# Kernel optimization log

Hardware: AMD Instinct MI355X
Metric: run time of the kernel (lower is better)

## Reference

```python
import jax, jax.numpy as jnp
import numpy as np

FACTOR = 5

def setup_inputs() -> dict:
    key = jax.random.key(0)
    k1, k2, k3, k4 = jax.random.split(key, 4)
    B, L, H, D = 4, 2048, 8, 64
    sample_k = min(FACTOR * int(np.ceil(np.log(L))), L)  # 40
    return {
        "queries": jax.random.normal(k1, (B, L, H, D), dtype=jnp.float32),
        "keys": jax.random.normal(k2, (B, L, H, D), dtype=jnp.float32),
        "values": jax.random.normal(k3, (B, L, H, D), dtype=jnp.float32),
        "index_sample": jax.random.randint(k4, (L, sample_k), 0, L, dtype=jnp.int32),
    }

def reference(queries, keys, values, index_sample):
    # [B, L, H, D] -> [B, H, L, D]
    Q = jnp.transpose(queries, (0, 2, 1, 3))
    K = jnp.transpose(keys, (0, 2, 1, 3))
    V = jnp.transpose(values, (0, 2, 1, 3))
    B, H, L_Q, D = Q.shape
    L_K = K.shape[2]
    u = min(FACTOR * int(np.ceil(np.log(L_Q))), L_Q)  # n_top

    # --- _prob_QK: sampled QK scores ---
    # K_sample: [B, H, L_Q, sample_k, D]
    K_sample = K[:, :, index_sample, :]
    # Q_K_sample[b,h,l,s] = Q[b,h,l,:] . K_sample[b,h,l,s,:]
    Q_K_sample = jnp.einsum('bhld,bhlsd->bhls', Q, K_sample)
    # sparsity measure M: max - mean over L_K
    M = Q_K_sample.max(axis=-1) - Q_K_sample.sum(axis=-1) / L_K  # [B,H,L_Q]
    _, M_top = jax.lax.top_k(M, u)  # [B,H,u]

    # reduced Q -> full scores against all keys
    Q_reduce = jnp.take_along_axis(Q, M_top[..., None], axis=2)  # [B,H,u,D]
    scores = jnp.einsum('bhud,bhkd->bhuk', Q_reduce, K)  # [B,H,u,L_K]
    scale = 1.0 / jnp.sqrt(jnp.asarray(D, dtype=scores.dtype))
    scores = scores * scale

    # --- initial context: mean of V over keys (mask_flag=False) ---
    V_mean = V.mean(axis=-2)  # [B,H,D]
    context = jnp.broadcast_to(V_mean[:, :, None, :], (B, H, L_Q, D))

    # --- update context at top-u query positions ---
    attn = jax.nn.softmax(scores, axis=-1)  # [B,H,u,L_K]
    ctx_top = jnp.einsum('bhuk,bhkd->bhud', attn, V)  # [B,H,u,D]
    b_idx = jnp.arange(B)[:, None, None]
    h_idx = jnp.arange(H)[None, :, None]
    context = context.at[b_idx, h_idx, M_top].set(ctx_top)
    return context  # [B, H, L_Q, D]
```

## Files before the change

### kernel.cpp

```cpp
#include <hip/hip_runtime.h>
#include <math.h>

#define LL 2048
#define HH 8
#define DD 64
#define SK 40
#define UU 40
#define SCALE 0.125f


__global__ __launch_bounds__(512) void k_m(
    const float* __restrict__ Q, const float* __restrict__ K,
    const int* __restrict__ idxs, float* __restrict__ Mout)
{
  int bx = blockIdx.x;
  int b = bx >> 11, l = bx & (LL - 1);
  int t = threadIdx.x;
  int h = t >> 6, lane = t & 63;
  int sg = lane >> 2, dg = lane & 3;

  const float* qrow = Q + (((size_t)(b * LL + l) * HH + h) << 6);
  float4 qv[4];
#pragma unroll
  for (int i = 0; i < 4; ++i)
    qv[i] = *(const float4*)(qrow + i * 16 + dg * 4);

  const int* ip = idxs + l * SK;
  float mx = -INFINITY, sum = 0.f;

#pragma unroll
  for (int c = 0; c < 3; ++c) {
    int s = c * 16 + sg;
    int idx = (s < SK) ? ip[s] : ip[0];
    const float* krow = K + (((size_t)(b * LL + idx) * HH + h) << 6);
    float p = 0.f;
#pragma unroll
    for (int i = 0; i < 4; ++i) {
      float4 kv = *(const float4*)(krow + i * 16 + dg * 4);
      p += qv[i].x * kv.x + qv[i].y * kv.y + qv[i].z * kv.z + qv[i].w * kv.w;
    }
    p += __shfl_xor(p, 1);
    p += __shfl_xor(p, 2);
    if (s < SK) { mx = fmaxf(mx, p); sum += p; }
  }
#pragma unroll
  for (int off = 4; off <= 32; off <<= 1) {
    mx = fmaxf(mx, __shfl_xor(mx, off));
    sum += __shfl_xor(sum, off);
  }
  if (lane == 0) Mout[(((size_t)b * HH + h) << 11) + l] = mx - sum * (1.0f / (float)LL);
}

__global__ __launch_bounds__(256) void k_topk(
    const float* __restrict__ Mv, int* __restrict__ Mtop)
{
  __shared__ float sv[LL];
  __shared__ float wm[4];
  __shared__ int wi[4];
  int bh = blockIdx.x;
  int t = threadIdx.x, w = t >> 6, ln = t & 63;
  for (int i = t; i < LL; i += 256) sv[i] = Mv[bh * LL + i];
  __syncthreads();
  for (int r = 0; r < UU; ++r) {
    float bv = -INFINITY; int bi = 0;
#pragma unroll
    for (int j = 0; j < 8; ++j) {
      int i = t + (j << 8);
      float v = sv[i];
      if (v > bv) { bv = v; bi = i; }
    }
#pragma unroll
    for (int off = 1; off < 64; off <<= 1) {
      float ov = __shfl_xor(bv, off);
      int oi = __shfl_xor(bi, off);
      if (ov > bv || (ov == bv && oi < bi)) { bv = ov; bi = oi; }
    }
    if (ln == 0) { wm[w] = bv; wi[w] = bi; }
    __syncthreads();
    if (t == 0) {
      float Bv = wm[0]; int Bi = wi[0];
#pragma unroll
      for (int k = 1; k < 4; ++k)
        if (wm[k] > Bv || (wm[k] == Bv && wi[k] < Bi)) { Bv = wm[k]; Bi = wi[k]; }
      Mtop[bh * UU + r] = Bi;
      sv[Bi] = -INFINITY;
    }
    __syncthreads();
  }
}

__global__ __launch_bounds__(256) void k_vpart(
    const float* __restrict__ V, float* __restrict__ part)
{
  int blk = blockIdx.x;
  int bh = blk >> 3, c = blk & 7;
  int b = bh >> 3, h = bh & 7;
  int t = threadIdx.x, d = t & 63, w = t >> 6;
  int l0 = (c << 8) + (w << 6);
  float a0 = 0, a1 = 0, a2 = 0, a3 = 0;
  for (int j = 0; j < 64; j += 4) {
    int l = l0 + j;
    a0 += V[(((size_t)(b * LL + l + 0) * HH + h) << 6) + d];
    a1 += V[(((size_t)(b * LL + l + 1) * HH + h) << 6) + d];
    a2 += V[(((size_t)(b * LL + l + 2) * HH + h) << 6) + d];
    a3 += V[(((size_t)(b * LL + l + 3) * HH + h) << 6) + d];
  }
  __shared__ float sm[4][64];
  sm[w][d] = a0 + a1 + a2 + a3;
  __syncthreads();
  if (t < 64) part[(blk << 6) + t] = sm[0][t] + sm[1][t] + sm[2][t] + sm[3][t];
}

__global__ __launch_bounds__(256) void k_vcomb(
    const float* __restrict__ part, float* __restrict__ Vmean)
{
  int e = blockIdx.x * 256 + threadIdx.x;
  int bh = e >> 6, d = e & 63;
  float s = 0;
#pragma unroll
  for (int c = 0; c < 8; ++c) s += part[(((bh << 3) + c) << 6) + d];
  Vmean[e] = s * (1.0f / (float)LL);
}

__global__ __launch_bounds__(256) void k_fill(
    const float4* __restrict__ Vmean4, float4* __restrict__ out4)
{
  int i = blockIdx.x * 256 + threadIdx.x;
  int d4 = i & 15;
  int bh = i >> 15;
  out4[i] = Vmean4[(bh << 4) + d4];
}

__global__ __launch_bounds__(512) void k_attn2(
    const float* __restrict__ Q, const float* __restrict__ K,
    const float* __restrict__ V, const int* __restrict__ Mtop,
    float* __restrict__ pm, float* __restrict__ pl, float4* __restrict__ pO4)
{
  __shared__ float4 Ks4[1024];
  __shared__ float Ps[8][256];
  __shared__ float4 Os4[4][2][4][16];
  __shared__ int gqi[8];

  int blk = blockIdx.x;
  int bh = blk / 40;
  int rem = blk % 40;
  int ch = rem / 5, rg = rem % 5;
  int b = bh >> 3, h = bh & 7;
  int t = threadIdx.x;
  int w = t >> 6, ln = t & 63;
  int l0 = ch << 8;

  if (t < 8) gqi[t] = Mtop[bh * UU + rg * 8 + t];
  __syncthreads();

  float4 qv[16];
  {
    const float4* qrow = (const float4*)(Q + (((size_t)(b * LL + gqi[w]) * HH + h) << 6));
#pragma unroll
    for (int i = 0; i < 16; ++i) qv[i] = qrow[i];
  }

  const float4* K4 = (const float4*)K;
  size_t kbase = ((size_t)(b * LL + l0) * HH + h) << 4;
  int col0 = t >> 4, d40 = t & 15;
  float4 g0, g1;
  g0 = K4[kbase + (size_t)(col0) * 128 + d40];
  g1 = K4[kbase + (size_t)(col0 + 32) * 128 + d40];

  float sc[4];
#pragma unroll
  for (int st = 0; st < 4; ++st) {
    __syncthreads();
    Ks4[col0 * 16 + (d40 ^ (col0 & 7))] = g0;
    Ks4[(col0 + 32) * 16 + (d40 ^ (col0 & 7))] = g1;
    float4 n0, n1;
    if (st < 3) {
      int lr = (st + 1) * 64;
      n0 = K4[kbase + (size_t)(lr + col0) * 128 + d40];
      n1 = K4[kbase + (size_t)(lr + col0 + 32) * 128 + d40];
    }
    __syncthreads();
    float s = 0.f;
#pragma unroll
    for (int d4 = 0; d4 < 16; ++d4) {
      float4 kv = Ks4[ln * 16 + (d4 ^ (ln & 7))];
      s += qv[d4].x * kv.x + qv[d4].y * kv.y + qv[d4].z * kv.z + qv[d4].w * kv.w;
    }
    sc[st] = s * SCALE;
    g0 = n0; g1 = n1;
  }

  float m = fmaxf(fmaxf(sc[0], sc[1]), fmaxf(sc[2], sc[3]));
#pragma unroll
  for (int off = 1; off < 64; off <<= 1) m = fmaxf(m, __shfl_xor(m, off));
  float lsum = 0.f;
#pragma unroll
  for (int st = 0; st < 4; ++st) {
    float p = __expf(sc[st] - m);
    Ps[w][st * 64 + ln] = p;
    lsum += p;
  }
#pragma unroll
  for (int off = 1; off < 64; off <<= 1) lsum += __shfl_xor(lsum, off);
  if (ln == 0) {
    int prow = bh * UU + rg * 8 + w;
    pm[prow * 8 + ch] = m;
    pl[prow * 8 + ch] = lsum;
  }
  __syncthreads();

  int rw = w >> 2, cq = w & 3;
  int cg = ln >> 4, d4 = ln & 15;
  float4 o0 = {0,0,0,0}, o1 = {0,0,0,0}, o2 = {0,0,0,0}, o3 = {0,0,0,0};
  const float4* vbase = K4;
  vbase = (const float4*)V + (((size_t)(b * LL + l0 + cq * 64) * HH + h) << 4) / 16 * 16;
  size_t vb = (((size_t)(b * LL + l0 + cq * 64) * HH + h) << 4);
  const float4* V4 = (const float4*)V;
#pragma unroll
  for (int i = 0; i < 16; ++i) {
    int c = i * 4 + cg;
    float4 v4 = V4[vb + (size_t)c * 128 + d4];
    float p0 = Ps[rw * 4 + 0][cq * 64 + c];
    float p1 = Ps[rw * 4 + 1][cq * 64 + c];
    float p2 = Ps[rw * 4 + 2][cq * 64 + c];
    float p3 = Ps[rw * 4 + 3][cq * 64 + c];
    o0.x += p0 * v4.x; o0.y += p0 * v4.y; o0.z += p0 * v4.z; o0.w += p0 * v4.w;
    o1.x += p1 * v4.x; o1.y += p1 * v4.y; o1.z += p1 * v4.z; o1.w += p1 * v4.w;
    o2.x += p2 * v4.x; o2.y += p2 * v4.y; o2.z += p2 * v4.z; o2.w += p2 * v4.w;
    o3.x += p3 * v4.x; o3.y += p3 * v4.y; o3.z += p3 * v4.z; o3.w += p3 * v4.w;
  }
#pragma unroll
  for (int off = 16; off <= 32; off <<= 1) {
    o0.x += __shfl_xor(o0.x, off); o0.y += __shfl_xor(o0.y, off);
    o0.z += __shfl_xor(o0.z, off); o0.w += __shfl_xor(o0.w, off);
    o1.x += __shfl_xor(o1.x, off); o1.y += __shfl_xor(o1.y, off);
    o1.z += __shfl_xor(o1.z, off); o1.w += __shfl_xor(o1.w, off);
    o2.x += __shfl_xor(o2.x, off); o2.y += __shfl_xor(o2.y, off);
    o2.z += __shfl_xor(o2.z, off); o2.w += __shfl_xor(o2.w, off);
    o3.x += __shfl_xor(o3.x, off); o3.y += __shfl_xor(o3.y, off);
    o3.z += __shfl_xor(o3.z, off); o3.w += __shfl_xor(o3.w, off);
  }
  if (cg == 0) {
    Os4[cq][rw][0][d4] = o0;
    Os4[cq][rw][1][d4] = o1;
    Os4[cq][rw][2][d4] = o2;
    Os4[cq][rw][3][d4] = o3;
  }
  __syncthreads();

  if (t < 128) {
    int r = t >> 4, dd = t & 15;
    float4 a = Os4[0][r >> 2][r & 3][dd];
    float4 bq = Os4[1][r >> 2][r & 3][dd];
    float4 cc = Os4[2][r >> 2][r & 3][dd];
    float4 dq = Os4[3][r >> 2][r & 3][dd];
    float4 s;
    s.x = a.x + bq.x + cc.x + dq.x;
    s.y = a.y + bq.y + cc.y + dq.y;
    s.z = a.z + bq.z + cc.z + dq.z;
    s.w = a.w + bq.w + cc.w + dq.w;
    int prow = bh * UU + rg * 8 + r;
    pO4[(prow * 8 + ch) * 16 + dd] = s;
  }
}

__global__ __launch_bounds__(256) void k_comb(
    const float* __restrict__ pm, const float* __restrict__ pl,
    const float* __restrict__ pO, const int* __restrict__ Mtop,
    float* __restrict__ out)
{
  int row = blockIdx.x * 4 + (threadIdx.x >> 6);
  int ln = threadIdx.x & 63;
  int bh = row / UU, r40 = row % UU;
  float mm[8];
#pragma unroll
  for (int c = 0; c < 8; ++c) mm[c] = pm[row * 8 + c];
  float ms = mm[0];
#pragma unroll
  for (int c = 1; c < 8; ++c) ms = fmaxf(ms, mm[c]);
  float wsum = 0.f, o = 0.f;
#pragma unroll
  for (int c = 0; c < 8; ++c) {
    float wc = __expf(mm[c] - ms);
    wsum += wc * pl[row * 8 + c];
    o += wc * pO[(row * 8 + c) * 64 + ln];
  }
  int gq = Mtop[bh * UU + r40];
  out[(((size_t)bh * LL + gq) << 6) + ln] = o / wsum;
}

extern "C" void kernel_launch(void* const* d_in, const int* in_sizes, int n_in,
                              void* d_out, int out_size, void* d_ws, size_t ws_size,
                              hipStream_t stream)
{
  (void)in_sizes; (void)n_in; (void)out_size; (void)ws_size;
  const float* Q = (const float*)d_in[0];
  const float* K = (const float*)d_in[1];
  const float* V = (const float*)d_in[2];
  const int* idxs = (const int*)d_in[3];
  float* out = (float*)d_out;

  float* wsf = (float*)d_ws;
  float* M     = wsf;
  float* part  = wsf + 65536;
  float* Vmean = wsf + 81920;
  int*   Mtop  = (int*)(wsf + 83968);
  float* pm    = wsf + 85248;
  float* pl    = wsf + 95488;
  float* pO    = wsf + 105728;

  k_m    <<<8192, 512, 0, stream>>>(Q, K, idxs, M);
  k_topk <<<32,   256, 0, stream>>>(M, Mtop);
  k_vpart<<<256,  256, 0, stream>>>(V, part);
  k_vcomb<<<8,    256, 0, stream>>>(part, Vmean);
  k_fill <<<4096, 256, 0, stream>>>((const float4*)Vmean, (float4*)out);
  k_attn2<<<1280, 512, 0, stream>>>(Q, K, V, Mtop, pm, pl, (float4*)pO);
  k_comb <<<320,  256, 0, stream>>>(pm, pl, pO, Mtop, out);
}
```

Measured before the change: 217.5 us.

## Remap block indices for XCD L2 locality, fuse V-mean into fill, use 32-bit indexing

```diff
diff --git a/kernel.cpp b/kernel.cpp
--- a/kernel.cpp
+++ b/kernel.cpp
@@ -14,30 +14,36 @@
     const int* __restrict__ idxs, float* __restrict__ Mout)
 {
   int bx = blockIdx.x;
-  int b = bx >> 11, l = bx & (LL - 1);
+  int xcd = bx & 7, slot = bx >> 3;
+  int b = xcd >> 1;
+  int l = ((xcd & 1) << 10) | slot;
   int t = threadIdx.x;
   int h = t >> 6, lane = t & 63;
   int sg = lane >> 2, dg = lane & 3;
 
-  const float* qrow = Q + (((size_t)(b * LL + l) * HH + h) << 6);
+  int kb = b << 20;
+  int qoff = kb + (l << 9) + (h << 6) + (dg << 2);
   float4 qv[4];
 #pragma unroll
   for (int i = 0; i < 4; ++i)
-    qv[i] = *(const float4*)(qrow + i * 16 + dg * 4);
+    qv[i] = *(const float4*)(Q + qoff + i * 16);
 
   const int* ip = idxs + l * SK;
+  int kconst = kb + (h << 6) + (dg << 2);
   float mx = -INFINITY, sum = 0.f;
 
 #pragma unroll
   for (int c = 0; c < 3; ++c) {
     int s = c * 16 + sg;
-    int idx = (s < SK) ? ip[s] : ip[0];
-    const float* krow = K + (((size_t)(b * LL + idx) * HH + h) << 6);
     float p = 0.f;
-#pragma unroll
-    for (int i = 0; i < 4; ++i) {
-      float4 kv = *(const float4*)(krow + i * 16 + dg * 4);
-      p += qv[i].x * kv.x + qv[i].y * kv.y + qv[i].z * kv.z + qv[i].w * kv.w;
+    if (s < SK) {
+      int koff = kconst + (ip[s] << 9);
+      const float* krow = K + koff;
+#pragma unroll
+      for (int i = 0; i < 4; ++i) {
+        float4 kv = *(const float4*)(krow + i * 16);
+        p += qv[i].x * kv.x + qv[i].y * kv.y + qv[i].z * kv.z + qv[i].w * kv.w;
+      }
     }
     p += __shfl_xor(p, 1);
     p += __shfl_xor(p, 2);
@@ -48,7 +54,7 @@
     mx = fmaxf(mx, __shfl_xor(mx, off));
     sum += __shfl_xor(sum, off);
   }
-  if (lane == 0) Mout[(((size_t)b * HH + h) << 11) + l] = mx - sum * (1.0f / (float)LL);
+  if (lane == 0) Mout[((b * HH + h) << 11) + l] = mx - sum * (1.0f / (float)LL);
 }
 
 __global__ __launch_bounds__(256) void k_topk(
@@ -97,13 +103,13 @@
   int b = bh >> 3, h = bh & 7;
   int t = threadIdx.x, d = t & 63, w = t >> 6;
   int l0 = (c << 8) + (w << 6);
+  int base = (b << 20) + (l0 << 9) + (h << 6) + d;
   float a0 = 0, a1 = 0, a2 = 0, a3 = 0;
   for (int j = 0; j < 64; j += 4) {
-    int l = l0 + j;
-    a0 += V[(((size_t)(b * LL + l + 0) * HH + h) << 6) + d];
-    a1 += V[(((size_t)(b * LL + l + 1) * HH + h) << 6) + d];
-    a2 += V[(((size_t)(b * LL + l + 2) * HH + h) << 6) + d];
-    a3 += V[(((size_t)(b * LL + l + 3) * HH + h) << 6) + d];
+    a0 += V[base + ((j + 0) << 9)];
+    a1 += V[base + ((j + 1) << 9)];
+    a2 += V[base + ((j + 2) << 9)];
+    a3 += V[base + ((j + 3) << 9)];
   }
   __shared__ float sm[4][64];
   sm[w][d] = a0 + a1 + a2 + a3;
@@ -111,24 +117,26 @@
   if (t < 64) part[(blk << 6) + t] = sm[0][t] + sm[1][t] + sm[2][t] + sm[3][t];
 }
 
-__global__ __launch_bounds__(256) void k_vcomb(
-    const float* __restrict__ part, float* __restrict__ Vmean)
-{
-  int e = blockIdx.x * 256 + threadIdx.x;
-  int bh = e >> 6, d = e & 63;
-  float s = 0;
-#pragma unroll
-  for (int c = 0; c < 8; ++c) s += part[(((bh << 3) + c) << 6) + d];
-  Vmean[e] = s * (1.0f / (float)LL);
-}
-
 __global__ __launch_bounds__(256) void k_fill(
-    const float4* __restrict__ Vmean4, float4* __restrict__ out4)
+    const float4* __restrict__ part4, float4* __restrict__ out4)
 {
   int i = blockIdx.x * 256 + threadIdx.x;
-  int d4 = i & 15;
   int bh = i >> 15;
-  out4[i] = Vmean4[(bh << 4) + d4];
+  __shared__ float4 vm[16];
+  if (threadIdx.x < 16) {
+    int d4 = threadIdx.x;
+    float4 s = {0, 0, 0, 0};
+#pragma unroll
+    for (int c = 0; c < 8; ++c) {
+      float4 p = part4[((bh << 3) + c) * 16 + d4];
+      s.x += p.x; s.y += p.y; s.z += p.z; s.w += p.w;
+    }
+    const float inv = 1.0f / (float)LL;
+    s.x *= inv; s.y *= inv; s.z *= inv; s.w *= inv;
+    vm[d4] = s;
+  }
+  __syncthreads();
+  out4[i] = vm[i & 15];
 }
 
 __global__ __launch_bounds__(512) void k_attn2(
@@ -141,10 +149,10 @@
   __shared__ float4 Os4[4][2][4][16];
   __shared__ int gqi[8];
 
-  int blk = blockIdx.x;
-  int bh = blk / 40;
-  int rem = blk % 40;
-  int ch = rem / 5, rg = rem % 5;
+  int bx = blockIdx.x;
+  int ch = bx & 7;
+  int slot = bx >> 3;
+  int bh = slot / 5, rg = slot % 5;
   int b = bh >> 3, h = bh & 7;
   int t = threadIdx.x;
   int w = t >> 6, ln = t & 63;
@@ -155,29 +163,29 @@
 
   float4 qv[16];
   {
-    const float4* qrow = (const float4*)(Q + (((size_t)(b * LL + gqi[w]) * HH + h) << 6));
+    const float4* qrow = (const float4*)Q + (((b << 11) + gqi[w]) << 7) + (h << 4);
 #pragma unroll
     for (int i = 0; i < 16; ++i) qv[i] = qrow[i];
   }
 
   const float4* K4 = (const float4*)K;
-  size_t kbase = ((size_t)(b * LL + l0) * HH + h) << 4;
+  int kbase = (((b << 11) + l0) << 7) + (h << 4);
   int col0 = t >> 4, d40 = t & 15;
-  float4 g0, g1;
-  g0 = K4[kbase + (size_t)(col0) * 128 + d40];
-  g1 = K4[kbase + (size_t)(col0 + 32) * 128 + d40];
+  int sw0 = col0 * 16 + (d40 ^ (col0 & 7));
+  float4 g0 = K4[kbase + col0 * 128 + d40];
+  float4 g1 = K4[kbase + (col0 + 32) * 128 + d40];
 
   float sc[4];
 #pragma unroll
   for (int st = 0; st < 4; ++st) {
     __syncthreads();
-    Ks4[col0 * 16 + (d40 ^ (col0 & 7))] = g0;
-    Ks4[(col0 + 32) * 16 + (d40 ^ (col0 & 7))] = g1;
+    Ks4[sw0] = g0;
+    Ks4[sw0 + 512] = g1;
     float4 n0, n1;
     if (st < 3) {
       int lr = (st + 1) * 64;
-      n0 = K4[kbase + (size_t)(lr + col0) * 128 + d40];
-      n1 = K4[kbase + (size_t)(lr + col0 + 32) * 128 + d40];
+      n0 = K4[kbase + (lr + col0) * 128 + d40];
+      n1 = K4[kbase + (lr + col0 + 32) * 128 + d40];
     }
     __syncthreads();
     float s = 0.f;
@@ -212,14 +220,12 @@
   int rw = w >> 2, cq = w & 3;
   int cg = ln >> 4, d4 = ln & 15;
   float4 o0 = {0,0,0,0}, o1 = {0,0,0,0}, o2 = {0,0,0,0}, o3 = {0,0,0,0};
-  const float4* vbase = K4;
-  vbase = (const float4*)V + (((size_t)(b * LL + l0 + cq * 64) * HH + h) << 4) / 16 * 16;
-  size_t vb = (((size_t)(b * LL + l0 + cq * 64) * HH + h) << 4);
+  int vb = (((b << 11) + l0 + cq * 64) << 7) + (h << 4);
   const float4* V4 = (const float4*)V;
 #pragma unroll
   for (int i = 0; i < 16; ++i) {
     int c = i * 4 + cg;
-    float4 v4 = V4[vb + (size_t)c * 128 + d4];
+    float4 v4 = V4[vb + c * 128 + d4];
     float p0 = Ps[rw * 4 + 0][cq * 64 + c];
     float p1 = Ps[rw * 4 + 1][cq * 64 + c];
     float p2 = Ps[rw * 4 + 2][cq * 64 + c];
@@ -286,7 +292,7 @@
     o += wc * pO[(row * 8 + c) * 64 + ln];
   }
   int gq = Mtop[bh * UU + r40];
-  out[(((size_t)bh * LL + gq) << 6) + ln] = o / wsum;
+  out[((bh * LL + gq) << 6) + ln] = o / wsum;
 }
 
 extern "C" void kernel_launch(void* const* d_in, const int* in_sizes, int n_in,
@@ -303,7 +309,6 @@
   float* wsf = (float*)d_ws;
   float* M     = wsf;
   float* part  = wsf + 65536;
-  float* Vmean = wsf + 81920;
   int*   Mtop  = (int*)(wsf + 83968);
   float* pm    = wsf + 85248;
   float* pl    = wsf + 95488;
@@ -312,8 +317,7 @@
   k_m    <<<8192, 512, 0, stream>>>(Q, K, idxs, M);
   k_topk <<<32,   256, 0, stream>>>(M, Mtop);
   k_vpart<<<256,  256, 0, stream>>>(V, part);
-  k_vcomb<<<8,    256, 0, stream>>>(part, Vmean);
-  k_fill <<<4096, 256, 0, stream>>>((const float4*)Vmean, (float4*)out);
+  k_fill <<<4096, 256, 0, stream>>>((const float4*)part, (float4*)out);
   k_attn2<<<1280, 512, 0, stream>>>(Q, K, V, Mtop, pm, pl, (float4*)pO);
   k_comb <<<320,  256, 0, stream>>>(pm, pl, pO, Mtop, out);
 }
```

After: 215.7 us. Within noise of the previous version (-0.8%).
